# Optimization experiments

Hardware: AMD Instinct MI355X
Metric: run time of the kernel (lower is better)

## Reference

```python
import jax, jax.numpy as jnp
import numpy as np

N, D, V = 4096, 512, 100000


def setup_inputs() -> dict:
    key = jax.random.key(0)
    k1, k2, k3 = jax.random.split(key, 3)
    x = jax.random.normal(k1, (N, D), dtype=jnp.float32)
    lb = jax.random.randint(k2, (N,), 0, V, dtype=jnp.int64)
    W = jax.random.normal(k3, (V, D), dtype=jnp.float32) * 0.02
    b = jnp.zeros((V,), dtype=jnp.float32)
    return {"x": x, "lb": lb, "W": W, "b": b}


def reference(x, lb, W, b):
    # fc: logits[N, V] = x @ W^T + b
    logits = jnp.einsum('nd,vd->nv', x, W) + b
    # numerically-stable softmax cross-entropy, mean reduction
    logz = jax.nn.logsumexp(logits, axis=-1)               # [N]
    tgt = jnp.take_along_axis(logits, lb[:, None], axis=-1)[:, 0]  # [N]
    loss = jnp.mean(logz - tgt)
    return loss
```

## Files before the change

kernel.cpp:

```cpp
#include <hip/hip_runtime.h>
#include <hip/hip_bf16.h>
#include <math.h>


#define N_ROWS 4096
#define DIM    512
#define VOCAB  100000
#define NTILES 782
#define VPAD   (NTILES * 128)
#define SPLITS 32
#define TPS    25
#define XELEMS (N_ROWS * DIM)
#define WVALID ((size_t)VOCAB * DIM)
#define WBYTES ((size_t)VPAD * DIM)
#define TILEB  (128 * DIM)

#define LOG2E 1.44269504088896340736f

typedef __attribute__((ext_vector_type(4))) int   i32x4;
typedef __attribute__((ext_vector_type(8))) int   i32x8;
typedef __attribute__((ext_vector_type(4))) float f32x4;

#define WAITV(n) asm volatile("s_waitcnt vmcnt(" #n ")" ::: "memory")
#define BARRIER_PIN()                         \
  do {                                        \
    __builtin_amdgcn_s_barrier();             \
    __builtin_amdgcn_sched_barrier(0);        \
  } while (0)


__device__ __forceinline__ void gload_lds16(const char* g, char* l) {
  __builtin_amdgcn_global_load_lds(
      (const __attribute__((address_space(1))) unsigned int*)g,
      (__attribute__((address_space(3))) unsigned int*)l, 16, 0, 0);
}

__device__ __forceinline__ int pack4_fp8(float4 f, float sc) {
  int p = __builtin_amdgcn_cvt_pk_fp8_f32(f.x * sc, f.y * sc, 0, false);
  p = __builtin_amdgcn_cvt_pk_fp8_f32(f.z * sc, f.w * sc, p, true);
  return p;
}

__device__ __forceinline__ i32x8 frag32(const char* base) {
  i32x4 lo = *(const i32x4*)(base);
  i32x4 hi = *(const i32x4*)(base + 1024);
  return (i32x8){lo.x, lo.y, lo.z, lo.w, hi.x, hi.y, hi.z, hi.w};
}

template <bool FIRST>
__device__ __forceinline__ void mfma_step(const i32x8 a0, const i32x8 a1,
                                          const char* fB, f32x4 acc[2][8]) {
  __builtin_amdgcn_s_setprio(1);
#pragma unroll
  for (int j = 0; j < 8; ++j) {
    const i32x8 bf = frag32(fB + j * 2048);
    acc[0][j] = __builtin_amdgcn_mfma_scale_f32_16x16x128_f8f6f4(
        a0, bf, FIRST ? (f32x4){0.f, 0.f, 0.f, 0.f} : acc[0][j], 0, 0, 0, 127, 0, 122);
    acc[1][j] = __builtin_amdgcn_mfma_scale_f32_16x16x128_f8f6f4(
        a1, bf, FIRST ? (f32x4){0.f, 0.f, 0.f, 0.f} : acc[1][j], 0, 0, 0, 127, 0, 122);
  }
  __builtin_amdgcn_s_setprio(0);
}


__global__ __launch_bounds__(256) void cvt_kernel(const float* __restrict__ x,
                                                  const float* __restrict__ W,
                                                  char* __restrict__ out8) {
  const size_t e = ((size_t)blockIdx.x * 256 + threadIdx.x) * 16;
  int4 o;
  if (e < (size_t)XELEMS) {
    const float4* s = (const float4*)(x + e);
    o.x = pack4_fp8(s[0], LOG2E); o.y = pack4_fp8(s[1], LOG2E);
    o.z = pack4_fp8(s[2], LOG2E); o.w = pack4_fp8(s[3], LOG2E);
  } else if (e - XELEMS < WVALID) {
    const float4* s = (const float4*)(W + (e - XELEMS));
    o.x = pack4_fp8(s[0], 32.f); o.y = pack4_fp8(s[1], 32.f);
    o.z = pack4_fp8(s[2], 32.f); o.w = pack4_fp8(s[3], 32.f);
  } else {
    o.x = 0; o.y = 0; o.z = 0; o.w = 0;
  }
  *(int4*)(out8 + e) = o;
}


__global__ __launch_bounds__(256) void tgt_kernel(const float* __restrict__ x,
                                                  const int* __restrict__ lb,
                                                  const float* __restrict__ W,
                                                  const float* __restrict__ bias,
                                                  float* __restrict__ tgt) {
  const int wv = threadIdx.x >> 6;
  const int lane = threadIdx.x & 63;
  const int row = blockIdx.x * 4 + wv;
  const int t = lb[row];
  const float* xr = x + (size_t)row * DIM;
  const float* wr = W + (size_t)t * DIM;
  float s = 0.f;
#pragma unroll
  for (int i = 0; i < 8; ++i) s += xr[lane + i * 64] * wr[lane + i * 64];
#pragma unroll
  for (int m = 32; m; m >>= 1) s += __shfl_xor(s, m);
  if (lane == 0) tgt[row] = s + bias[t];
}


__global__ __launch_bounds__(256, 2) void lse_kernel(const char* __restrict__ xb,
                                                     const char* __restrict__ wb,
                                                     const float* __restrict__ bias,
                                                     float* __restrict__ spart) {
  __shared__ __align__(16) char ldsB[4][16384];
  __shared__ float ldsBias[TPS * 128];

  const int d = blockIdx.x;
  const int s     = 2 * (d & 7) + ((d >> 3) & 1) + 16 * (d >> 9);
  const int mtile = (d >> 4) & 31;

  const int m0 = mtile * 128;
  const int t0 = s * TPS;
  const int t1 = (t0 + TPS < NTILES) ? (t0 + TPS) : NTILES;
  const int NT = t1 - t0;

  const int tid  = threadIdx.x;
  const int lane = tid & 63;
  const int wv   = tid >> 6;
  const int fr   = lane & 15;
  const int fq   = lane >> 4;

  i32x8 Aa[2][4];
  {
    const char* ax = xb + (size_t)(m0 + 32 * wv + fr) * DIM + fq * 32;
#pragma unroll
    for (int i = 0; i < 2; ++i)
#pragma unroll
      for (int ks = 0; ks < 4; ++ks) {
        const char* p = ax + i * (16 * DIM) + ks * 128;
        i32x4 lo = *(const i32x4*)p;
        i32x4 hi = *(const i32x4*)(p + 16);
        Aa[i][ks] = (i32x8){lo.x, lo.y, lo.z, lo.w, hi.x, hi.y, hi.z, hi.w};
      }
  }

  for (int c = tid; c < NT * 128; c += 256) {
    const int col = t0 * 128 + c;
    ldsBias[c] = (col < VOCAB) ? bias[col] * LOG2E : -INFINITY;
  }
  __syncthreads();
  asm volatile("s_waitcnt vmcnt(0)" ::: "memory");
  __builtin_amdgcn_sched_barrier(0);

  const size_t bRowOff = (size_t)(32 * wv + fr) * DIM + fq * 32;
  char* const dB0 = &ldsB[0][wv * 4096];
  char* const dB1 = &ldsB[1][wv * 4096];
  char* const dB2 = &ldsB[2][wv * 4096];
  char* const dB3 = &ldsB[3][wv * 4096];

  auto stageB = [&](const char* src, char* dst) {
    gload_lds16(src,                 dst);
    gload_lds16(src + 16,            dst + 1024);
    gload_lds16(src + 16 * DIM,      dst + 2048);
    gload_lds16(src + 16 * DIM + 16, dst + 3072);
  };

  float S[2][4];
#pragma unroll
  for (int i = 0; i < 2; ++i)
#pragma unroll
    for (int r = 0; r < 4; ++r) S[i][r] = 0.f;

  f32x4 acc[2][8];

  const char* fB0 = &ldsB[0][lane * 16];
  const char* fB1 = &ldsB[1][lane * 16];
  const char* fB2 = &ldsB[2][lane * 16];
  const char* fB3 = &ldsB[3][lane * 16];

  auto epilogue = [&](int ti) {
    const float* bT = &ldsBias[ti * 128];
    float badd[8];
#pragma unroll
    for (int j = 0; j < 8; ++j) badd[j] = bT[16 * j + fr];
#pragma unroll
    for (int i = 0; i < 2; ++i)
#pragma unroll
      for (int r = 0; r < 4; ++r) {
        float sum = 0.f;
#pragma unroll
        for (int j = 0; j < 8; ++j)
          sum += __builtin_amdgcn_exp2f(acc[i][j][r] + badd[j]);
        S[i][r] += sum;
      }
  };

  const char* wt = wb + (size_t)t0 * TILEB + bRowOff;

  stageB(wt,       dB0);
  stageB(wt + 128, dB1);
  stageB(wt + 256, dB2);

  for (int tt = t0; tt < t1 - 1; ++tt, wt += TILEB) {
    WAITV(8); BARRIER_PIN();
    stageB(wt + 384, dB3);
    mfma_step<true>(Aa[0][0], Aa[1][0], fB0, acc);

    WAITV(8); BARRIER_PIN();
    stageB(wt + TILEB, dB0);
    mfma_step<false>(Aa[0][1], Aa[1][1], fB1, acc);

    WAITV(8); BARRIER_PIN();
    stageB(wt + TILEB + 128, dB1);
    mfma_step<false>(Aa[0][2], Aa[1][2], fB2, acc);

    WAITV(8); BARRIER_PIN();
    stageB(wt + TILEB + 256, dB2);
    mfma_step<false>(Aa[0][3], Aa[1][3], fB3, acc);

    epilogue(tt - t0);
  }

  {
    WAITV(8); BARRIER_PIN();
    stageB(wt + 384, dB3);
    mfma_step<true>(Aa[0][0], Aa[1][0], fB0, acc);

    WAITV(8); BARRIER_PIN();
    mfma_step<false>(Aa[0][1], Aa[1][1], fB1, acc);

    WAITV(4); BARRIER_PIN();
    mfma_step<false>(Aa[0][2], Aa[1][2], fB2, acc);

    WAITV(0); BARRIER_PIN();
    mfma_step<false>(Aa[0][3], Aa[1][3], fB3, acc);

    epilogue(NT - 1);
  }

#pragma unroll
  for (int i = 0; i < 2; ++i)
#pragma unroll
    for (int r = 0; r < 4; ++r) {
      float v = S[i][r];
      v += __shfl_xor(v, 1);
      v += __shfl_xor(v, 2);
      v += __shfl_xor(v, 4);
      v += __shfl_xor(v, 8);
      if (fr == 0) {
        const int row = m0 + 32 * wv + 16 * i + 4 * fq + r;
        spart[(size_t)row * SPLITS + s] = v;
      }
    }
}


__global__ __launch_bounds__(256) void combine_kernel(const float* __restrict__ spart,
                                                      const float* __restrict__ tgt,
                                                      float* __restrict__ out) {
  __shared__ float red[256];
  float local = 0.f;
  for (int r = threadIdx.x; r < N_ROWS; r += 256) {
    const float4* sp = (const float4*)(spart + (size_t)r * SPLITS);
    float st = 0.f;
#pragma unroll
    for (int i = 0; i < 8; ++i) { float4 v = sp[i]; st += (v.x + v.y) + (v.z + v.w); }
    local += __logf(st) - tgt[r];
  }
  red[threadIdx.x] = local;
  __syncthreads();
  for (int step = 128; step; step >>= 1) {
    if (threadIdx.x < step) red[threadIdx.x] += red[threadIdx.x + step];
    __syncthreads();
  }
  if (threadIdx.x == 0) out[0] = red[0] * (1.0f / (float)N_ROWS);
}


extern "C" void kernel_launch(void* const* d_in, const int* in_sizes, int n_in,
                              void* d_out, int out_size, void* d_ws, size_t ws_size,
                              hipStream_t stream) {
  const float* x  = (const float*)d_in[0];
  const int*   lb = (const int*)d_in[1];
  const float* W  = (const float*)d_in[2];
  const float* b  = (const float*)d_in[3];
  float* out = (float*)d_out;

  char* ws = (char*)d_ws;
  const size_t OFF_W   = (size_t)XELEMS;
  const size_t OFF_SP  = OFF_W + WBYTES;
  const size_t OFF_TGT = OFF_SP + (size_t)N_ROWS * SPLITS * 4;
  char*  xb    = ws;
  char*  wb    = ws + OFF_W;
  float* spart = (float*)(ws + OFF_SP);
  float* tgt   = (float*)(ws + OFF_TGT);

  cvt_kernel<<<13024, 256, 0, stream>>>(x, W, ws);
  tgt_kernel<<<1024, 256, 0, stream>>>(x, lb, W, b, tgt);
  lse_kernel<<<1024, 256, 0, stream>>>(xb, wb, b, spart);
  combine_kernel<<<1, 256, 0, stream>>>(spart, tgt, out);
}
```

Baseline: 586.3 us.

## Retile LSE GEMM to 2x2 wave grid with double-buffered K phases

Changes the wave layout from each wave owning 32 rows by 128 vocab columns to a 2x2 grid where each wave owns 64 rows by 64 columns. B fragments loaded from LDS are then reused across four row fragments instead of two, which cuts LDS read traffic per MFMA. The 4-stage pipeline with partial vmcnt waits becomes a 2-buffer scheme (two K-steps per phase) with full vmcnt(0) waits. A cross-wave LDS reduction is added at the end to merge the two column halves. The trade-off is less load/compute overlap, higher register pressure from 16 A fragments, and extra synchronization.

```diff
diff --git a/kernel.cpp b/kernel.cpp
--- a/kernel.cpp
+++ b/kernel.cpp
@@ -21,7 +21,7 @@
 typedef __attribute__((ext_vector_type(8))) int   i32x8;
 typedef __attribute__((ext_vector_type(4))) float f32x4;
 
-#define WAITV(n) asm volatile("s_waitcnt vmcnt(" #n ")" ::: "memory")
+#define WAITV0() asm volatile("s_waitcnt vmcnt(0)" ::: "memory")
 #define BARRIER_PIN()                         \
   do {                                        \
     __builtin_amdgcn_s_barrier();             \
@@ -45,21 +45,6 @@
   i32x4 lo = *(const i32x4*)(base);
   i32x4 hi = *(const i32x4*)(base + 1024);
   return (i32x8){lo.x, lo.y, lo.z, lo.w, hi.x, hi.y, hi.z, hi.w};
-}
-
-template <bool FIRST>
-__device__ __forceinline__ void mfma_step(const i32x8 a0, const i32x8 a1,
-                                          const char* fB, f32x4 acc[2][8]) {
-  __builtin_amdgcn_s_setprio(1);
-#pragma unroll
-  for (int j = 0; j < 8; ++j) {
-    const i32x8 bf = frag32(fB + j * 2048);
-    acc[0][j] = __builtin_amdgcn_mfma_scale_f32_16x16x128_f8f6f4(
-        a0, bf, FIRST ? (f32x4){0.f, 0.f, 0.f, 0.f} : acc[0][j], 0, 0, 0, 127, 0, 122);
-    acc[1][j] = __builtin_amdgcn_mfma_scale_f32_16x16x128_f8f6f4(
-        a1, bf, FIRST ? (f32x4){0.f, 0.f, 0.f, 0.f} : acc[1][j], 0, 0, 0, 127, 0, 122);
-  }
-  __builtin_amdgcn_s_setprio(0);
 }
 
 
@@ -107,7 +92,7 @@
                                                      const char* __restrict__ wb,
                                                      const float* __restrict__ bias,
                                                      float* __restrict__ spart) {
-  __shared__ __align__(16) char ldsB[4][16384];
+  __shared__ __align__(16) char ldsB[2][32768];
   __shared__ float ldsBias[TPS * 128];
 
   const int d = blockIdx.x;
@@ -122,20 +107,22 @@
   const int tid  = threadIdx.x;
   const int lane = tid & 63;
   const int wv   = tid >> 6;
+  const int rh   = wv >> 1;
+  const int ch   = wv & 1;
   const int fr   = lane & 15;
   const int fq   = lane >> 4;
 
-  i32x8 Aa[2][4];
+  i32x8 Aa[4][4];
   {
-    const char* ax = xb + (size_t)(m0 + 32 * wv + fr) * DIM + fq * 32;
-#pragma unroll
-    for (int i = 0; i < 2; ++i)
+    const char* ax = xb + (size_t)(m0 + 64 * rh + fr) * DIM + fq * 32;
+#pragma unroll
+    for (int rf = 0; rf < 4; ++rf)
 #pragma unroll
       for (int ks = 0; ks < 4; ++ks) {
-        const char* p = ax + i * (16 * DIM) + ks * 128;
+        const char* p = ax + rf * (16 * DIM) + ks * 128;
         i32x4 lo = *(const i32x4*)p;
         i32x4 hi = *(const i32x4*)(p + 16);
-        Aa[i][ks] = (i32x8){lo.x, lo.y, lo.z, lo.w, hi.x, hi.y, hi.z, hi.w};
+        Aa[rf][ks] = (i32x8){lo.x, lo.y, lo.z, lo.w, hi.x, hi.y, hi.z, hi.w};
       }
   }
 
@@ -144,109 +131,117 @@
     ldsBias[c] = (col < VOCAB) ? bias[col] * LOG2E : -INFINITY;
   }
   __syncthreads();
-  asm volatile("s_waitcnt vmcnt(0)" ::: "memory");
-  __builtin_amdgcn_sched_barrier(0);
-
-  const size_t bRowOff = (size_t)(32 * wv + fr) * DIM + fq * 32;
-  char* const dB0 = &ldsB[0][wv * 4096];
-  char* const dB1 = &ldsB[1][wv * 4096];
-  char* const dB2 = &ldsB[2][wv * 4096];
-  char* const dB3 = &ldsB[3][wv * 4096];
-
-  auto stageB = [&](const char* src, char* dst) {
-    gload_lds16(src,                 dst);
-    gload_lds16(src + 16,            dst + 1024);
-    gload_lds16(src + 16 * DIM,      dst + 2048);
-    gload_lds16(src + 16 * DIM + 16, dst + 3072);
+
+  auto stagePhase = [&](const char* tileSrc, int kp, char* buf) {
+#pragma unroll
+    for (int ks2 = 0; ks2 < 2; ++ks2) {
+      const char* s0 = tileSrc + (2 * kp + ks2) * 128 + fq * 32;
+#pragma unroll
+      for (int gg = 0; gg < 2; ++gg) {
+        const int g = 2 * wv + gg;
+        const char* src = s0 + (size_t)(16 * g + fr) * DIM;
+        char* dst = buf + ks2 * 16384 + g * 2048;
+        gload_lds16(src,      dst);
+        gload_lds16(src + 16, dst + 1024);
+      }
+    }
   };
 
-  float S[2][4];
-#pragma unroll
-  for (int i = 0; i < 2; ++i)
-#pragma unroll
-    for (int r = 0; r < 4; ++r) S[i][r] = 0.f;
-
-  f32x4 acc[2][8];
-
-  const char* fB0 = &ldsB[0][lane * 16];
-  const char* fB1 = &ldsB[1][lane * 16];
-  const char* fB2 = &ldsB[2][lane * 16];
-  const char* fB3 = &ldsB[3][lane * 16];
+  float S[4][4];
+#pragma unroll
+  for (int rf = 0; rf < 4; ++rf)
+#pragma unroll
+    for (int r = 0; r < 4; ++r) S[rf][r] = 0.f;
+
+  f32x4 acc[4][4];
+
+#define COMPUTE_PHASE(bufR, ksA, ksB, FIRSTF)                               \
+  {                                                                         \
+    __builtin_amdgcn_s_setprio(1);                                          \
+    _Pragma("unroll")                                                       \
+    for (int c = 0; c < 4; ++c) {                                           \
+      const char* fb = (bufR) + (4 * ch + c) * 2048 + lane * 16;            \
+      const i32x8 bf0 = frag32(fb);                                         \
+      const i32x8 bf1 = frag32(fb + 16384);                                 \
+      _Pragma("unroll")                                                     \
+      for (int rf = 0; rf < 4; ++rf) {                                      \
+        acc[rf][c] = __builtin_amdgcn_mfma_scale_f32_16x16x128_f8f6f4(      \
+            Aa[rf][ksA], bf0,                                               \
+            (FIRSTF) ? (f32x4){0.f, 0.f, 0.f, 0.f} : acc[rf][c],            \
+            0, 0, 0, 127, 0, 122);                                          \
+        acc[rf][c] = __builtin_amdgcn_mfma_scale_f32_16x16x128_f8f6f4(      \
+            Aa[rf][ksB], bf1, acc[rf][c], 0, 0, 0, 127, 0, 122);            \
+      }                                                                     \
+    }                                                                       \
+    __builtin_amdgcn_s_setprio(0);                                          \
+  }
 
   auto epilogue = [&](int ti) {
-    const float* bT = &ldsBias[ti * 128];
-    float badd[8];
-#pragma unroll
-    for (int j = 0; j < 8; ++j) badd[j] = bT[16 * j + fr];
-#pragma unroll
-    for (int i = 0; i < 2; ++i)
+    const float* bT = &ldsBias[ti * 128 + 64 * ch];
+    float badd[4];
+#pragma unroll
+    for (int c = 0; c < 4; ++c) badd[c] = bT[16 * c + fr];
+#pragma unroll
+    for (int rf = 0; rf < 4; ++rf)
 #pragma unroll
       for (int r = 0; r < 4; ++r) {
         float sum = 0.f;
 #pragma unroll
-        for (int j = 0; j < 8; ++j)
-          sum += __builtin_amdgcn_exp2f(acc[i][j][r] + badd[j]);
-        S[i][r] += sum;
+        for (int c = 0; c < 4; ++c)
+          sum += __builtin_amdgcn_exp2f(acc[rf][c][r] + badd[c]);
+        S[rf][r] += sum;
       }
   };
 
-  const char* wt = wb + (size_t)t0 * TILEB + bRowOff;
-
-  stageB(wt,       dB0);
-  stageB(wt + 128, dB1);
-  stageB(wt + 256, dB2);
-
-  for (int tt = t0; tt < t1 - 1; ++tt, wt += TILEB) {
-    WAITV(8); BARRIER_PIN();
-    stageB(wt + 384, dB3);
-    mfma_step<true>(Aa[0][0], Aa[1][0], fB0, acc);
-
-    WAITV(8); BARRIER_PIN();
-    stageB(wt + TILEB, dB0);
-    mfma_step<false>(Aa[0][1], Aa[1][1], fB1, acc);
-
-    WAITV(8); BARRIER_PIN();
-    stageB(wt + TILEB + 128, dB1);
-    mfma_step<false>(Aa[0][2], Aa[1][2], fB2, acc);
-
-    WAITV(8); BARRIER_PIN();
-    stageB(wt + TILEB + 256, dB2);
-    mfma_step<false>(Aa[0][3], Aa[1][3], fB3, acc);
+  const char* wt = wb + (size_t)t0 * TILEB;
+  stagePhase(wt, 0, ldsB[0]);
+
+  for (int tt = t0; tt < t1; ++tt, wt += TILEB) {
+    WAITV0(); BARRIER_PIN();
+    stagePhase(wt, 1, ldsB[1]);
+    __builtin_amdgcn_sched_barrier(0);
+    COMPUTE_PHASE(ldsB[0], 0, 1, true)
+
+    WAITV0(); BARRIER_PIN();
+    if (tt + 1 < t1) stagePhase(wt + TILEB, 0, ldsB[0]);
+    __builtin_amdgcn_sched_barrier(0);
+    COMPUTE_PHASE(ldsB[1], 2, 3, false)
 
     epilogue(tt - t0);
   }
 
-  {
-    WAITV(8); BARRIER_PIN();
-    stageB(wt + 384, dB3);
-    mfma_step<true>(Aa[0][0], Aa[1][0], fB0, acc);
-
-    WAITV(8); BARRIER_PIN();
-    mfma_step<false>(Aa[0][1], Aa[1][1], fB1, acc);
-
-    WAITV(4); BARRIER_PIN();
-    mfma_step<false>(Aa[0][2], Aa[1][2], fB2, acc);
-
-    WAITV(0); BARRIER_PIN();
-    mfma_step<false>(Aa[0][3], Aa[1][3], fB3, acc);
-
-    epilogue(NT - 1);
-  }
-
-#pragma unroll
-  for (int i = 0; i < 2; ++i)
-#pragma unroll
-    for (int r = 0; r < 4; ++r) {
-      float v = S[i][r];
-      v += __shfl_xor(v, 1);
-      v += __shfl_xor(v, 2);
-      v += __shfl_xor(v, 4);
-      v += __shfl_xor(v, 8);
-      if (fr == 0) {
-        const int row = m0 + 32 * wv + 16 * i + 4 * fq + r;
-        spart[(size_t)row * SPLITS + s] = v;
-      }
+  __syncthreads();
+  float* sc = (float*)ldsB;
+  if (ch == 1) {
+    float* base = sc + (size_t)(rh * 64 + lane) * 20;
+#pragma unroll
+    for (int rf = 0; rf < 4; ++rf)
+      *(float4*)(base + rf * 4) = (float4){S[rf][0], S[rf][1], S[rf][2], S[rf][3]};
+  }
+  __syncthreads();
+  if (ch == 0) {
+    const float* base = sc + (size_t)(rh * 64 + lane) * 20;
+#pragma unroll
+    for (int rf = 0; rf < 4; ++rf) {
+      const float4 v = *(const float4*)(base + rf * 4);
+      S[rf][0] += v.x; S[rf][1] += v.y; S[rf][2] += v.z; S[rf][3] += v.w;
     }
+#pragma unroll
+    for (int rf = 0; rf < 4; ++rf)
+#pragma unroll
+      for (int r = 0; r < 4; ++r) {
+        float v = S[rf][r];
+        v += __shfl_xor(v, 1);
+        v += __shfl_xor(v, 2);
+        v += __shfl_xor(v, 4);
+        v += __shfl_xor(v, 8);
+        if (fr == 0) {
+          const int row = m0 + 64 * rh + 16 * rf + 4 * fq + r;
+          spart[(size_t)row * SPLITS + s] = v;
+        }
+      }
+  }
+#undef COMPUTE_PHASE
 }
 
 
```

After: 557.8 us. 1.05x faster.
